# Optimization experiments

Hardware: AMD Instinct MI355X
Metric: run time of the kernel (lower is better)

The kernel has to match this reference:

```python
import jax, jax.numpy as jnp
import numpy as np

N_CODES = 1024
CODE_DIM = 256
DECAY = 0.99
EPS = 1e-05


def setup_inputs() -> dict:
    key = jax.random.key(0)
    k1, k2, k3, k4 = jax.random.split(key, 4)
    z = jax.random.normal(k1, (32, CODE_DIM, 32, 32), dtype=jnp.float32)
    embed = jax.random.normal(k2, (N_CODES, CODE_DIM), dtype=jnp.float32)
    cluster_size = jax.random.uniform(k3, (N_CODES,), dtype=jnp.float32)
    embed_avg = jax.random.normal(k4, (N_CODES, CODE_DIM), dtype=jnp.float32)
    return {"z": z, "embed": embed, "cluster_size": cluster_size, "embed_avg": embed_avg}


def reference(z, embed, cluster_size, embed_avg):
    B, D, H, W = z.shape
    K = embed.shape[0]
    # (B*H*W, D) tokens
    flat = jnp.transpose(z, (0, 2, 3, 1)).reshape(-1, D)
    distances = (
        jnp.sum(flat * flat, axis=1, keepdims=True)
        - 2.0 * flat @ embed.T
        + jnp.sum(embed * embed, axis=1)[None, :]
    )
    indices = jnp.argmin(distances, axis=1)  # (N,)
    z_q = embed[indices].reshape(B, H, W, D).transpose(0, 3, 1, 2)  # (B, D, H, W)

    # EMA codebook update (training mode), no onehot materialization
    cs = jax.ops.segment_sum(jnp.ones(flat.shape[0], dtype=flat.dtype), indices, num_segments=K)
    es = jax.ops.segment_sum(flat, indices, num_segments=K)
    new_cluster_size = cluster_size * DECAY + (1.0 - DECAY) * cs
    new_embed_avg = embed_avg * DECAY + (1.0 - DECAY) * es
    n = jnp.sum(new_cluster_size)
    cs_norm = (new_cluster_size + EPS) / (n + K * EPS) * n
    new_embed = new_embed_avg / cs_norm[:, None]

    # straight-through estimator
    z_q_st = z + jax.lax.stop_gradient(z_q - z)
    # torch: F.mse_loss(z.detach(), z_q) -> grads flow to z_q (codebook) only
    vq_loss = jnp.mean((jax.lax.stop_gradient(z) - z_q) ** 2)
    return (z_q_st, indices.reshape(B, H, W), vq_loss, new_embed, new_cluster_size, new_embed_avg)
```

## Files before the change

### kernel.cpp

```cpp
#include <hip/hip_runtime.h>
#include <stdint.h>

#define DECAY 0.99f
#define OMDECAY 0.01f
#define EPSV 1e-5f


typedef _Float16 half8 __attribute__((ext_vector_type(8)));
typedef float floatx4 __attribute__((ext_vector_type(4)));

typedef __attribute__((address_space(1))) const uint32_t gu32;
typedef __attribute__((address_space(3))) uint32_t lu32;

__device__ __forceinline__ void gld16(uint32_t* l, const uint32_t* g) {
    __builtin_amdgcn_global_load_lds((gu32*)g, (lu32*)l, 16, 0, 0);
}

__device__ __forceinline__ uint32_t pack_hl(float v) {
    _Float16 h = (_Float16)v;
    _Float16 lo = (_Float16)(v - (float)h);
    return (uint32_t)__builtin_bit_cast(unsigned short, h) |
           ((uint32_t)__builtin_bit_cast(unsigned short, lo) << 16);
}

__device__ __forceinline__ unsigned int encf(float s) {
    unsigned int b = __builtin_bit_cast(unsigned int, s);
    return (b & 0x80000000u) ? ~b : (b | 0x80000000u);
}

__global__ void prep_fused(const float* __restrict__ z,
                           uint32_t* __restrict__ A_hi32,
                           uint32_t* __restrict__ A_lo32,
                           const float* __restrict__ embed,
                           unsigned short* __restrict__ B_hi16,
                           unsigned short* __restrict__ B_lo16,
                           float* __restrict__ enorm,
                           float* __restrict__ cs ,
                           uint32_t* __restrict__ b64i) {
    __shared__ uint32_t sp[32 * 258];
    const int bx = blockIdx.x;
    const int tid = threadIdx.x;
    const int lane = tid & 63;
    const int wv = tid >> 6;

    if (bx < 1024) {
        const int t0  = bx * 32;
        const int b   = t0 >> 10;
        const int hw0 = t0 & 1023;
        const int l32 = lane & 31;
        const int dh  = lane >> 5;
        for (int dp = wv; dp < 128; dp += 4) {
            int dd = dp * 2 + dh;
            float v = z[b * 262144 + dd * 1024 + hw0 + l32];
            sp[l32 * 258 + dd] = pack_hl(v);
        }
        __syncthreads();
        for (int r = wv; r < 32; r += 4) {
#pragma unroll
            for (int h2 = 0; h2 < 2; ++h2) {
                int dpair = h2 * 64 + lane;
                uint32_t u0 = sp[r * 258 + 2 * dpair];
                uint32_t u1 = sp[r * 258 + 2 * dpair + 1];
                A_hi32[(t0 + r) * 128 + dpair] = (u0 & 0xffffu) | (u1 << 16);
                A_lo32[(t0 + r) * 128 + dpair] = (u0 >> 16) | (u1 & 0xffff0000u);
            }
        }
    } else {
        float* ws4 = (float*)sp;
        const int k = bx - 1024;
        int idx = k * 256 + tid;
        float v = embed[idx];
        _Float16 h = (_Float16)v;
        _Float16 lo = (_Float16)(v - (float)h);
        B_hi16[idx] = __builtin_bit_cast(unsigned short, h);
        B_lo16[idx] = __builtin_bit_cast(unsigned short, lo);
        float s = v * v;
        for (int off = 32; off > 0; off >>= 1) s += __shfl_down(s, off);
        if (lane == 0) ws4[wv] = s;
        __syncthreads();
        if (tid == 0) enorm[k] = ws4[0] + ws4[1] + ws4[2] + ws4[3];
        if (k < 256) b64i[k * 256 + tid] = 0xFFFFFFFFu;
        if (k == 0) {
            for (int i = tid; i < 2048; i += 256) cs[i] = 0.f;
        }
    }
}

__global__ __launch_bounds__(256, 2) void vq_mfma(
    const uint32_t* __restrict__ A_hi32,
    const uint32_t* __restrict__ A_lo32,
    const uint32_t* __restrict__ B_hi32,
    const uint32_t* __restrict__ B_lo32,
    const float* __restrict__ enorm,
    unsigned long long* __restrict__ best64)
{
    __shared__ __align__(16) _Float16 Abuf[2][2][4096];

    const int lane = threadIdx.x & 63;
    const int w    = threadIdx.x >> 6;
    const int q    = lane >> 4;
    const int c16  = lane & 15;
    const int bb   = blockIdx.x;
    const int xcd  = bb & 7;
    const int slot = bb >> 3;
    const int g    = (slot >> 2) * 8 + xcd;
    const int cq   = slot & 3;
    const int t0   = g * 128;
    const int cb   = cq * 256;
    const int lane4 = lane >> 2;
    const int dd8s  = ((lane & 3) ^ ((lane >> 3) & 3)) * 8;
    const int qs    = q ^ ((c16 >> 1) & 3);

    const uint32_t* const sA = (w >> 1) ? A_lo32 : A_hi32;
    const int r16b = (w & 1) * 4;

    float en[4];
    const uint32_t* bph[4];
    const uint32_t* bpl[4];
#pragma unroll
    for (int j = 0; j < 4; ++j) {
        const int code = cb + w * 64 + j * 16 + c16;
        en[j]  = enorm[code];
        bph[j] = B_hi32 + code * 128 + q * 4;
        bpl[j] = B_lo32 + code * 128 + q * 4;
    }

    floatx4 acc[8][4];
#pragma unroll
    for (int i = 0; i < 8; ++i)
#pragma unroll
        for (int j = 0; j < 4; ++j)
            acc[i][j] = (floatx4){0.f, 0.f, 0.f, 0.f};

    half8 bh[2][4], bl[2][4];

    auto STAGE_A = [&](int step) {
        uint32_t* dst = (uint32_t*)(&Abuf[step & 1][w >> 1][0]);
        const int srcoff = (step * 32 + dd8s) >> 1;
#pragma unroll
        for (int s = 0; s < 4; ++s) {
            const int r16 = r16b + s;
            gld16(dst + r16 * 256, sA + (t0 + r16 * 16 + lane4) * 128 + srcoff);
        }
    };
    auto LOAD_B = [&](int step, half8* h, half8* l) {
#pragma unroll
        for (int j = 0; j < 4; ++j) {
            h[j] = *(const half8*)(bph[j] + step * 16);
            l[j] = *(const half8*)(bpl[j] + step * 16);
        }
    };

    STAGE_A(0);
    LOAD_B(0, bh[0], bl[0]);

#pragma unroll
    for (int dc = 0; dc < 8; ++dc) {
        if (dc < 7) {
            STAGE_A(dc + 1);
            LOAD_B(dc + 1, bh[(dc + 1) & 1], bl[(dc + 1) & 1]);
            asm volatile("s_waitcnt vmcnt(12)" ::: "memory");
        } else {
            asm volatile("s_waitcnt vmcnt(0)" ::: "memory");
        }
        __builtin_amdgcn_s_barrier();
        asm volatile("" ::: "memory");

        const _Float16* pH = &Abuf[dc & 1][0][0];
        const _Float16* pL = &Abuf[dc & 1][1][0];
        __builtin_amdgcn_s_setprio(1);
#pragma unroll
        for (int i = 0; i < 8; ++i) {
            const int off = (i * 16 + c16) * 32 + qs * 8;
            half8 aH = *(const half8*)(pH + off);
            half8 aL = *(const half8*)(pL + off);
#pragma unroll
            for (int j = 0; j < 4; ++j) {
                acc[i][j] = __builtin_amdgcn_mfma_f32_16x16x32_f16(aH, bh[dc & 1][j], acc[i][j], 0, 0, 0);
                acc[i][j] = __builtin_amdgcn_mfma_f32_16x16x32_f16(aH, bl[dc & 1][j], acc[i][j], 0, 0, 0);
                acc[i][j] = __builtin_amdgcn_mfma_f32_16x16x32_f16(aL, bh[dc & 1][j], acc[i][j], 0, 0, 0);
            }
        }
        __builtin_amdgcn_s_setprio(0);
        asm volatile("" ::: "memory");
        if (dc < 7) __builtin_amdgcn_s_barrier();
    }

    unsigned long long best[32];
#pragma unroll
    for (int sl = 0; sl < 32; ++sl) best[sl] = ~0ULL;
#pragma unroll
    for (int j = 0; j < 4; ++j) {
        const unsigned int code = (unsigned int)(cb + w * 64 + j * 16 + c16);
        const float enj = en[j];
#pragma unroll
        for (int i = 0; i < 8; ++i)
#pragma unroll
            for (int r = 0; r < 4; ++r) {
                float sc = enj - 2.0f * acc[i][j][r];
                unsigned long long key =
                    ((unsigned long long)encf(sc) << 32) | code;
                int sl = i * 4 + r;
                if (key < best[sl]) best[sl] = key;
            }
    }
#pragma unroll
    for (int sl = 0; sl < 32; ++sl) {
        unsigned long long v = best[sl];
#pragma unroll
        for (int mm = 1; mm < 16; mm <<= 1) {
            unsigned long long o = __shfl_xor(v, mm);
            if (o < v) v = o;
        }
        if (c16 == (sl & 15)) {
            int tok = t0 + (sl >> 2) * 16 + q * 4 + (sl & 3);
            atomicMin(&best64[tok], v);
        }
    }
}

__global__ __launch_bounds__(256) void merge_zq(
    const unsigned long long* __restrict__ best64,
    const float* __restrict__ z,
    const float* __restrict__ embed,
    float* __restrict__ out_zq,
    float* __restrict__ out_idx,
    float* __restrict__ cs,
    float* __restrict__ loss_sum)
{
    __shared__ int sidx[128];
    const int tid = threadIdx.x;
    const int lane = tid & 63;
    const int w = tid >> 6;
    const int t0 = blockIdx.x * 128;

    if (tid < 128) {
        int bi = (int)(unsigned int)(best64[t0 + tid] & 0xffffffffULL);
        sidx[tid] = bi;
        out_idx[t0 + tid] = (float)bi;
        atomicAdd(&cs[bi], 1.0f);
    }
    __syncthreads();

    const int b_idx = t0 >> 10;
    const int hw0   = t0 & 1023;
    const int zbase = b_idx * 262144 + hw0;
    const int ka = sidx[lane];
    const int kb = sidx[lane + 64];
    float lsum = 0.f;
    for (int d = w; d < 256; d += 4) {
        float zv0 = z[zbase + d * 1024 + lane];
        float zv1 = z[zbase + d * 1024 + lane + 64];
        float e0 = embed[ka * 256 + d];
        float e1 = embed[kb * 256 + d];
        out_zq[zbase + d * 1024 + lane]      = zv0 + (e0 - zv0);
        out_zq[zbase + d * 1024 + lane + 64] = zv1 + (e1 - zv1);
        float d0f = zv0 - e0, d1f = zv1 - e1;
        lsum += d0f * d0f + d1f * d1f;
    }
    for (int off = 32; off > 0; off >>= 1) lsum += __shfl_down(lsum, off);
    if (lane == 0) atomicAdd(loss_sum, lsum);
}

__global__ void vq_finalize_small(const float* __restrict__ cluster_size,
                                  const float* __restrict__ cs,
                                  const float* __restrict__ loss_sum,
                                  float* __restrict__ out_loss,
                                  float* __restrict__ out_ncs,
                                  float* __restrict__ csnorm,
                                  int* __restrict__ offsets,
                                  int* __restrict__ cursor)
{
    __shared__ float wsum[16];
    __shared__ float wncs[16];
    __shared__ float stot[1];
    const int k = threadIdx.x;
    const int lane = k & 63;
    const int wv = k >> 6;
    float cnt = cs[k];
    float ncs = cluster_size[k] * DECAY + OMDECAY * cnt;
    out_ncs[k] = ncs;
    float sc = cnt;
#pragma unroll
    for (int d = 1; d < 64; d <<= 1) {
        float up = __shfl_up(sc, d);
        if (lane >= d) sc += up;
    }
    if (lane == 63) wsum[wv] = sc;
    float ns = ncs;
    for (int off = 32; off > 0; off >>= 1) ns += __shfl_down(ns, off);
    if (lane == 0) wncs[wv] = ns;
    __syncthreads();
    if (wv == 0) {
        float v = (lane < 16) ? wsum[lane] : 0.f;
#pragma unroll
        for (int d = 1; d < 16; d <<= 1) {
            float up = __shfl_up(v, d);
            if (lane >= d) v += up;
        }
        if (lane < 16) wsum[lane] = v;
    } else if (wv == 1) {
        float t = (lane < 16) ? wncs[lane] : 0.f;
        for (int off = 32; off > 0; off >>= 1) t += __shfl_down(t, off);
        if (lane == 0) stot[0] = t;
    }
    __syncthreads();
    float incl = sc + (wv ? wsum[wv - 1] : 0.f);
    int excl = __float2int_rn(incl - cnt);
    offsets[k] = excl;
    cursor[k]  = excl;
    float n = stot[0];
    csnorm[k] = (ncs + EPSV) / (n + 1024.0f * EPSV) * n;
    if (k == 0) out_loss[0] = loss_sum[0] / 8388608.0f;
}

__global__ void scatter_perm(const float* __restrict__ out_idx,
                             int* __restrict__ cursor,
                             int* __restrict__ perm,
                             float* __restrict__ es)
{
    int t = blockIdx.x * 256 + threadIdx.x;
#pragma unroll
    for (int i = 0; i < 8; ++i) es[t + i * 32768] = 0.f;
    int code = (int)out_idx[t];
    int pos = atomicAdd(&cursor[code], 1);
    perm[pos] = t;
}

__global__ void es_sum(const uint32_t* __restrict__ A_hi32,
                       const uint32_t* __restrict__ A_lo32,
                       const int* __restrict__ perm,
                       const float* __restrict__ out_idx,
                       float* __restrict__ es)
{
    __shared__ int sperm[32];
    __shared__ int scode[32];
    const int base = blockIdx.x * 32;
    const int tid = threadIdx.x;
    const int j = tid & 127;
    const uint32_t* __restrict__ A = (tid >> 7) ? A_lo32 : A_hi32;
    if (tid < 32) {
        int t = perm[base + tid];
        sperm[tid] = t;
        scode[tid] = (int)out_idx[t];
    }
    __syncthreads();

    float s0 = 0.f, s1 = 0.f;
    int cur = scode[0];
    uint32_t pu[2];
    pu[0] = A[sperm[0] * 128 + j];
    pu[1] = A[sperm[1] * 128 + j];
#pragma unroll
    for (int i = 0; i < 32; ++i) {
        uint32_t u = pu[i & 1];
        if (i + 2 < 32) pu[i & 1] = A[sperm[i + 2] * 128 + j];
        int code = scode[i];
        if (code != cur) {
            atomicAdd(&es[cur * 256 + 2 * j],     s0);
            atomicAdd(&es[cur * 256 + 2 * j + 1], s1);
            s0 = 0.f; s1 = 0.f; cur = code;
        }
        s0 += (float)__builtin_bit_cast(_Float16, (unsigned short)(u & 0xffffu));
        s1 += (float)__builtin_bit_cast(_Float16, (unsigned short)(u >> 16));
    }
    atomicAdd(&es[cur * 256 + 2 * j],     s0);
    atomicAdd(&es[cur * 256 + 2 * j + 1], s1);
}

__global__ void finalize_embed(const float* __restrict__ embed_avg,
                               const float* __restrict__ es,
                               const float* __restrict__ csnorm,
                               float* __restrict__ out_embed,
                               float* __restrict__ out_nea)
{
    int idx = blockIdx.x * 256 + threadIdx.x;
    int k = idx >> 8;
    float nea = embed_avg[idx] * DECAY + OMDECAY * es[idx];
    out_nea[idx] = nea;
    out_embed[idx] = nea / csnorm[k];
}

extern "C" void kernel_launch(void* const* d_in, const int* in_sizes, int n_in,
                              void* d_out, int out_size, void* d_ws, size_t ws_size,
                              hipStream_t stream) {
    const float* z            = (const float*)d_in[0];
    const float* embed        = (const float*)d_in[1];
    const float* cluster_size = (const float*)d_in[2];
    const float* embed_avg    = (const float*)d_in[3];
    float* out = (float*)d_out;
    uint32_t* ws32 = (uint32_t*)d_ws;

    uint32_t* B_hi32 = ws32 + 0;
    uint32_t* B_lo32 = ws32 + 131072;
    uint32_t* A_hi32 = ws32 + 262144;
    uint32_t* A_lo32 = ws32 + 4456448;
    int* perm        = (int*)(ws32 + 8650752);
    int* offsets     = (int*)(ws32 + 8683520);
    int* cursor      = (int*)(ws32 + 8684544);
    float* cs        = (float*)(ws32 + 8912896);
    float* loss_sum  = (float*)(ws32 + 8913920);
    float* enorm     = (float*)(ws32 + 8914944);
    float* csnorm    = (float*)(ws32 + 8915968);
    float* es        = (float*)(ws32 + 0);
    unsigned long long* best64 = (unsigned long long*)(out + 8421378);

    prep_fused<<<2048, 256, 0, stream>>>(z, A_hi32, A_lo32, embed,
                                         (unsigned short*)B_hi32,
                                         (unsigned short*)B_lo32, enorm, cs,
                                         (uint32_t*)best64);
    vq_mfma<<<1024, 256, 0, stream>>>(A_hi32, A_lo32, B_hi32, B_lo32, enorm, best64);
    merge_zq<<<256, 256, 0, stream>>>(best64, z, embed,
                                      out, out + 8388608, cs, loss_sum);
    vq_finalize_small<<<1, 1024, 0, stream>>>(cluster_size, cs, loss_sum,
                                              out + 8421376, out + 8683521, csnorm,
                                              offsets, cursor);
    scatter_perm<<<128, 256, 0, stream>>>(out + 8388608, cursor, perm, es);
    es_sum<<<1024, 256, 0, stream>>>(A_hi32, A_lo32, perm, out + 8388608, es);
    finalize_embed<<<1024, 256, 0, stream>>>(embed_avg, es, csnorm,
                                             out + 8421377, out + 8684545);
}
```

Before: 247.2 us.

## Compute VQ loss from stashed token norms and argmin scores; retile codebook layout

Token squared norms are computed during the prep transpose and stashed in the index output slot. The merge kernel then derives each token's loss as ||z||^2 plus the decoded best score, so it no longer reads z, and it writes z_q straight from embed rows using float4 loads and smaller blocks. The fp16 hi/lo codebook is also stored in a tiled layout so MFMA B loads for each step are contiguous. Risks: the loss now depends on the precision of the split-fp16 score rather than an exact fp32 difference, and z_q_st is written as e rather than z+(e-z).

```diff
diff --git a/kernel.cpp b/kernel.cpp
--- a/kernel.cpp
+++ b/kernel.cpp
@@ -26,6 +26,10 @@
 __device__ __forceinline__ unsigned int encf(float s) {
     unsigned int b = __builtin_bit_cast(unsigned int, s);
     return (b & 0x80000000u) ? ~b : (b | 0x80000000u);
+}
+__device__ __forceinline__ float decf(unsigned int u) {
+    unsigned int b = (u & 0x80000000u) ? (u ^ 0x80000000u) : ~u;
+    return __builtin_bit_cast(float, b);
 }
 
 __global__ void prep_fused(const float* __restrict__ z,
@@ -36,8 +40,10 @@
                            unsigned short* __restrict__ B_lo16,
                            float* __restrict__ enorm,
                            float* __restrict__ cs ,
-                           uint32_t* __restrict__ b64i) {
+                           uint32_t* __restrict__ b64i,
+                           float* __restrict__ znstash) {
     __shared__ uint32_t sp[32 * 258];
+    __shared__ float znacc[4][32];
     const int bx = blockIdx.x;
     const int tid = threadIdx.x;
     const int lane = tid & 63;
@@ -49,12 +55,19 @@
         const int hw0 = t0 & 1023;
         const int l32 = lane & 31;
         const int dh  = lane >> 5;
+        float zn = 0.f;
         for (int dp = wv; dp < 128; dp += 4) {
             int dd = dp * 2 + dh;
             float v = z[b * 262144 + dd * 1024 + hw0 + l32];
             sp[l32 * 258 + dd] = pack_hl(v);
-        }
+            zn += v * v;
+        }
+        zn += __shfl_xor(zn, 32);
+        if (lane < 32) znacc[wv][lane] = zn;
         __syncthreads();
+        if (tid < 32)
+            znstash[t0 + tid] = znacc[0][tid] + znacc[1][tid] +
+                                znacc[2][tid] + znacc[3][tid];
         for (int r = wv; r < 32; r += 4) {
 #pragma unroll
             for (int h2 = 0; h2 < 2; ++h2) {
@@ -68,12 +81,16 @@
     } else {
         float* ws4 = (float*)sp;
         const int k = bx - 1024;
-        int idx = k * 256 + tid;
-        float v = embed[idx];
+        const int d = tid;
+        float v = embed[k * 256 + d];
         _Float16 h = (_Float16)v;
         _Float16 lo = (_Float16)(v - (float)h);
-        B_hi16[idx] = __builtin_bit_cast(unsigned short, h);
-        B_lo16[idx] = __builtin_bit_cast(unsigned short, lo);
+        const int c16 = k & 15, cg = k >> 4;
+        const int dc = d >> 5, dl = d & 31;
+        const int qq = dl >> 3, dw = (dl & 7) >> 1, hl = d & 1;
+        const int us = ((cg * 8 + dc) * 256 + c16 * 16 + qq * 4 + dw) * 2 + hl;
+        B_hi16[us] = __builtin_bit_cast(unsigned short, h);
+        B_lo16[us] = __builtin_bit_cast(unsigned short, lo);
         float s = v * v;
         for (int off = 32; off > 0; off >>= 1) s += __shfl_down(s, off);
         if (lane == 0) ws4[wv] = s;
@@ -121,8 +138,9 @@
     for (int j = 0; j < 4; ++j) {
         const int code = cb + w * 64 + j * 16 + c16;
         en[j]  = enorm[code];
-        bph[j] = B_hi32 + code * 128 + q * 4;
-        bpl[j] = B_lo32 + code * 128 + q * 4;
+        const int cgj = (cb >> 4) + w * 4 + j;
+        bph[j] = B_hi32 + cgj * 2048 + c16 * 16 + q * 4;
+        bpl[j] = B_lo32 + cgj * 2048 + c16 * 16 + q * 4;
     }
 
     floatx4 acc[8][4];
@@ -146,8 +164,8 @@
     auto LOAD_B = [&](int step, half8* h, half8* l) {
 #pragma unroll
         for (int j = 0; j < 4; ++j) {
-            h[j] = *(const half8*)(bph[j] + step * 16);
-            l[j] = *(const half8*)(bpl[j] + step * 16);
+            h[j] = *(const half8*)(bph[j] + step * 256);
+            l[j] = *(const half8*)(bpl[j] + step * 256);
         }
     };
 
@@ -221,24 +239,29 @@
 
 __global__ __launch_bounds__(256) void merge_zq(
     const unsigned long long* __restrict__ best64,
-    const float* __restrict__ z,
     const float* __restrict__ embed,
     float* __restrict__ out_zq,
-    float* __restrict__ out_idx,
+    float* __restrict__ out_idx ,
     float* __restrict__ cs,
     float* __restrict__ loss_sum)
 {
-    __shared__ int sidx[128];
+    __shared__ int sidx[64];
     const int tid = threadIdx.x;
     const int lane = tid & 63;
     const int w = tid >> 6;
-    const int t0 = blockIdx.x * 128;
-
-    if (tid < 128) {
-        int bi = (int)(unsigned int)(best64[t0 + tid] & 0xffffffffULL);
-        sidx[tid] = bi;
-        out_idx[t0 + tid] = (float)bi;
-        atomicAdd(&cs[bi], 1.0f);
+    const int t0 = blockIdx.x * 64;
+
+    if (tid < 64) {
+        unsigned long long key = best64[t0 + tid];
+        int code = (int)(unsigned int)(key & 0xffffffffULL);
+        float sc = decf((unsigned int)(key >> 32));
+        float zn = out_idx[t0 + tid];
+        sidx[tid] = code;
+        out_idx[t0 + tid] = (float)code;
+        atomicAdd(&cs[code], 1.0f);
+        float val = zn + sc;
+        for (int off = 32; off > 0; off >>= 1) val += __shfl_down(val, off);
+        if (lane == 0) atomicAdd(loss_sum, val);
     }
     __syncthreads();
 
@@ -246,20 +269,14 @@
     const int hw0   = t0 & 1023;
     const int zbase = b_idx * 262144 + hw0;
     const int ka = sidx[lane];
-    const int kb = sidx[lane + 64];
-    float lsum = 0.f;
-    for (int d = w; d < 256; d += 4) {
-        float zv0 = z[zbase + d * 1024 + lane];
-        float zv1 = z[zbase + d * 1024 + lane + 64];
-        float e0 = embed[ka * 256 + d];
-        float e1 = embed[kb * 256 + d];
-        out_zq[zbase + d * 1024 + lane]      = zv0 + (e0 - zv0);
-        out_zq[zbase + d * 1024 + lane + 64] = zv1 + (e1 - zv1);
-        float d0f = zv0 - e0, d1f = zv1 - e1;
-        lsum += d0f * d0f + d1f * d1f;
-    }
-    for (int off = 32; off > 0; off >>= 1) lsum += __shfl_down(lsum, off);
-    if (lane == 0) atomicAdd(loss_sum, lsum);
+    const float* erow = embed + ka * 256;
+    for (int dq = w; dq < 64; dq += 4) {
+        float4 e4 = *(const float4*)(erow + dq * 4);
+        out_zq[zbase + (dq * 4 + 0) * 1024 + lane] = e4.x;
+        out_zq[zbase + (dq * 4 + 1) * 1024 + lane] = e4.y;
+        out_zq[zbase + (dq * 4 + 2) * 1024 + lane] = e4.z;
+        out_zq[zbase + (dq * 4 + 3) * 1024 + lane] = e4.w;
+    }
 }
 
 __global__ void vq_finalize_small(const float* __restrict__ cluster_size,
@@ -404,13 +421,14 @@
     float* csnorm    = (float*)(ws32 + 8915968);
     float* es        = (float*)(ws32 + 0);
     unsigned long long* best64 = (unsigned long long*)(out + 8421378);
+    float* znstash = out + 8388608;
 
     prep_fused<<<2048, 256, 0, stream>>>(z, A_hi32, A_lo32, embed,
                                          (unsigned short*)B_hi32,
                                          (unsigned short*)B_lo32, enorm, cs,
-                                         (uint32_t*)best64);
+                                         (uint32_t*)best64, znstash);
     vq_mfma<<<1024, 256, 0, stream>>>(A_hi32, A_lo32, B_hi32, B_lo32, enorm, best64);
-    merge_zq<<<256, 256, 0, stream>>>(best64, z, embed,
+    merge_zq<<<512, 256, 0, stream>>>(best64, embed,
                                       out, out + 8388608, cs, loss_sum);
     vq_finalize_small<<<1, 1024, 0, stream>>>(cluster_size, cs, loss_sum,
                                               out + 8421376, out + 8683521, csnorm,
```

After: 230.5 us. -6.7%, faster.
